# Kernel tuning notes

Hardware: AMD Instinct MI355X
Metric: run time of the kernel (lower is better)

## Reference

```python
import jax, jax.numpy as jnp
import numpy as np

C = 256
DEPTH = 4
GRIDS = [(128, 128), (128, 128), (128, 128)]
B = 2
N = 32768


def _ln_c(x, g, b):
    # LayerNorm over channel dim of [B, C, N] (myLayerNorm transposes to [B,N,C])
    m = x.mean(axis=1, keepdims=True)
    v = ((x - m) ** 2).mean(axis=1, keepdims=True)
    return (x - m) * jax.lax.rsqrt(v + 1e-5) * g[None, :, None] + b[None, :, None]


def _bn_train(x, g, b):
    # BatchNorm1d (training-mode batch stats) over [B, C, L]
    m = x.mean(axis=(0, 2), keepdims=True)
    v = ((x - m) ** 2).mean(axis=(0, 2), keepdims=True)
    return (x - m) * jax.lax.rsqrt(v + 1e-5) * g[None, :, None] + b[None, :, None]


def _dwconv3(x, w, b):
    # depthwise 3x3 conv, SAME padding; x [B,C,H,W], w [C,3,3]
    out = jax.lax.conv_general_dilated(x, w[:, None, :, :], (1, 1), 'SAME',
                                       feature_group_count=C,
                                       dimension_numbers=('NCHW', 'OIHW', 'NCHW'))
    return out + b[None, :, None, None]


def setup_inputs() -> dict:
    key = jax.random.key(0)
    ks = jax.random.split(key, 20)
    tokens = jax.random.normal(ks[0], (B, C, N), jnp.float32)
    hw = GRIDS[0][0] * GRIDS[0][1]
    cell_ind = jax.random.randint(ks[1], (B, 3, N), 0, hw)
    occupied_cell = jnp.ones((B, N), jnp.float32)

    def p(k, shape, scale=0.05):
        return scale * jax.random.normal(k, shape, jnp.float32)

    inp = dict(tokens=tokens, cell_ind=cell_ind, occupied_cell=occupied_cell)
    inp['smix_ln_g'] = 1.0 + p(ks[2], (DEPTH, C))
    inp['smix_ln_b'] = p(ks[3], (DEPTH, C))
    inp['ffn_w1'] = p(ks[4], (DEPTH, C, 3, 3), 0.2)
    inp['ffn_b1'] = p(ks[5], (DEPTH, C))
    inp['ffn_w2'] = p(ks[6], (DEPTH, C, 3, 3), 0.2)
    inp['ffn_b2'] = p(ks[7], (DEPTH, C))
    inp['att_scale'] = 1.0 + p(ks[8], (DEPTH, C))
    inp['att_bn_g'] = 1.0 + p(ks[9], (DEPTH, C))
    inp['att_bn_b'] = p(ks[10], (DEPTH, C))
    inp['cmix_ln_g'] = 1.0 + p(ks[11], (DEPTH, C))
    inp['cmix_ln_b'] = p(ks[12], (DEPTH, C))
    inp['cmix_w1'] = p(ks[13], (DEPTH, C, C), 1.0 / float(np.sqrt(C)))
    inp['cmix_b1'] = p(ks[14], (DEPTH, C))
    inp['cmix_w2'] = p(ks[15], (DEPTH, C, C), 1.0 / float(np.sqrt(C)))
    inp['cmix_b2'] = p(ks[16], (DEPTH, C))
    inp['cmix_scale'] = p(ks[17], (DEPTH, C), 0.1)
    return inp


def _forward(tokens, occupied_cell, cell_ind,
             smix_ln_g, smix_ln_b, ffn_w1, ffn_b1, ffn_w2, ffn_b2,
             att_scale, att_bn_g, att_bn_b,
             cmix_ln_g, cmix_ln_b, cmix_w1, cmix_b1, cmix_w2, cmix_b2, cmix_scale):
    Bx, Cx, Nx = tokens.shape
    bidx = jnp.arange(Bx)[:, None]
    # build_proj_matrix equivalent: per-point 1/(points-in-cell) weights + clamped indices
    sp = []
    for g in range(len(GRIDS)):
        HW = GRIDS[g][0] * GRIDS[g][1]
        ci = jnp.clip(cell_ind[:, g], 0, HW - 1)
        # inflate^T @ occupied: per-cell occupied count (occupied^2 per point)
        counts = jnp.zeros((Bx, HW), tokens.dtype).at[bidx, ci].add(occupied_cell * occupied_cell)
        # inflate @ counts: per-point count of points sharing its cell
        npp = occupied_cell * jnp.take_along_axis(counts, ci, axis=1)
        sp.append((ci, occupied_cell / (npp + 1e-6)))
    skip = [jnp.zeros(GRIDS[g], tokens.dtype) for g in range(len(GRIDS))]
    for d in range(DEPTH):
        g = d % len(GRIDS)
        H, W = GRIDS[g]
        HW = H * W
        ci, wpt = sp[g]
        # --- SpatialMix ---
        r = _ln_c(tokens, smix_ln_g[d], smix_ln_b[d]) * wpt[:, None, :]
        grid = jnp.zeros((Bx, Cx, HW), tokens.dtype).at[
            jnp.arange(Bx)[:, None, None], jnp.arange(Cx)[None, :, None], ci[:, None, :]].add(r)
        grid = grid.reshape(Bx, Cx, H, W) + skip[g]
        plane = _dwconv3(jax.nn.relu(_dwconv3(grid, ffn_w1[d], ffn_b1[d])), ffn_w2[d], ffn_b2[d])
        rflat = plane.reshape(Bx, Cx, HW)
        att = jax.nn.sigmoid(_bn_train(rflat * att_scale[d][None, :, None], att_bn_g[d], att_bn_b[d]))
        rflat = att * rflat
        r = jnp.take_along_axis(rflat, jnp.broadcast_to(ci[:, None, :], (Bx, Cx, Nx)), axis=2)
        tokens = tokens + r
        skip[g] = plane
        # --- ChannelMix ---
        h = _ln_c(tokens, cmix_ln_g[d], cmix_ln_b[d])
        h = jnp.einsum('oc,bcn->bon', cmix_w1[d], h) + cmix_b1[d][None, :, None]
        h = jnp.einsum('oc,bcn->bon', cmix_w2[d], jax.nn.relu(h)) + cmix_b2[d][None, :, None]
        tokens = tokens + h * cmix_scale[d][None, :, None]
    return tokens


def reference(tokens, cell_ind, occupied_cell,
              smix_ln_g, smix_ln_b, ffn_w1, ffn_b1, ffn_w2, ffn_b2,
              att_scale, att_bn_g, att_bn_b,
              cmix_ln_g, cmix_ln_b, cmix_w1, cmix_b1, cmix_w2, cmix_b2, cmix_scale):
    return _forward(tokens, occupied_cell, cell_ind,
                    smix_ln_g, smix_ln_b, ffn_w1, ffn_b1, ffn_w2, ffn_b2,
                    att_scale, att_bn_g, att_bn_b,
                    cmix_ln_g, cmix_ln_b, cmix_w1, cmix_b1, cmix_w2, cmix_b2, cmix_scale)
```

## Files before the change

kernel.cpp:

```cpp
#include <hip/hip_runtime.h>
#include <hip/hip_bf16.h>
#include <hip/hip_fp16.h>

#define Cc 256
#define Nn 32768
#define HWc 16384
#define Bb 2

typedef float floatx4 __attribute__((ext_vector_type(4)));
typedef short bf16x8 __attribute__((ext_vector_type(8)));
typedef unsigned short ushort8v __attribute__((ext_vector_type(8)));
typedef unsigned short ushort4v __attribute__((ext_vector_type(4)));

__device__ __forceinline__ unsigned short f2b(float f){
    unsigned u = __float_as_uint(f);
    u += 0x7fff + ((u >> 16) & 1);
    return (unsigned short)(u >> 16);
}
__device__ __forceinline__ float b2f(unsigned short h){
    return __uint_as_float(((unsigned)h) << 16);
}
__device__ __forceinline__ unsigned short f2h(float f){
    return __half_as_ushort(__float2half(f));
}
__device__ __forceinline__ float h2f(unsigned short h){
    return __half2float(__ushort_as_half(h));
}

__global__ __launch_bounds__(256) void k_count(const int* __restrict__ ci,
                                               const float* __restrict__ occ,
                                               float* __restrict__ fcounts,
                                               int* __restrict__ icounts){
    int idx = blockIdx.x*256 + threadIdx.x;
    if (idx >= Bb*3*Nn) return;
    int n = idx & (Nn-1);
    int bg = idx >> 15;
    int b = bg / 3;
    int cell = min(max(ci[idx], 0), HWc-1);
    float o = occ[(b<<15) + n];
    atomicAdd(&fcounts[(bg<<14) + cell], o*o);
    atomicAdd(&icounts[(bg<<14) + cell], 1);
}

__global__ __launch_bounds__(256) void k_wpt(const int* __restrict__ ci,
                                             const float* __restrict__ occ,
                                             const float* __restrict__ fcounts,
                                             float* __restrict__ wpt){
    int idx = blockIdx.x*256 + threadIdx.x;
    if (idx >= Bb*3*Nn) return;
    int n = idx & (Nn-1);
    int bg = idx >> 15;
    int b = bg / 3;
    int cell = min(max(ci[idx], 0), HWc-1);
    float o = occ[(b<<15) + n];
    float cnt = fcounts[(bg<<14) + cell];
    wpt[idx] = o / (o*cnt + 1e-6f);
}

__global__ __launch_bounds__(256) void k_scan(const int* __restrict__ ic,
                                              int* __restrict__ starts,
                                              int* __restrict__ cursor){
    __shared__ int part[256];
    int bg = blockIdx.x;
    int t = threadIdx.x;
    const int* cs = ic + (bg << 14);
    int base = t * 64;
    int s = 0;
    for (int i = 0; i < 64; ++i) s += cs[base + i];
    part[t] = s;
    __syncthreads();
    for (int off = 1; off < 256; off <<= 1){
        int v = (t >= off) ? part[t - off] : 0;
        __syncthreads();
        part[t] += v;
        __syncthreads();
    }
    int run = (t == 0) ? 0 : part[t - 1];
    int* st = starts + bg * (HWc + 1);
    int* cu = cursor + (bg << 14);
    for (int i = 0; i < 64; ++i){
        st[base + i] = run;
        cu[base + i] = run;
        run += cs[base + i];
    }
    if (t == 255) st[HWc] = run;
}

__global__ __launch_bounds__(256) void k_fill(const int* __restrict__ ci,
                                              int* __restrict__ cursor,
                                              int* __restrict__ plist){
    int idx = blockIdx.x*256 + threadIdx.x;
    if (idx >= Bb*3*Nn) return;
    int n = idx & (Nn-1);
    int bg = idx >> 15;
    int cell = min(max(ci[idx], 0), HWc-1);
    int pos = atomicAdd(&cursor[(bg<<14) + cell], 1);
    plist[(bg<<15) + pos] = n;
}

__global__ __launch_bounds__(256) void k_wcvt(const float* __restrict__ w1,
                                              const float* __restrict__ w2,
                                              unsigned short* __restrict__ W1b,
                                              unsigned short* __restrict__ W2b){
    int idx = blockIdx.x*256 + threadIdx.x;
    if (idx >= 4*Cc*Cc) return;
    W1b[idx] = f2b(w1[idx]);
    W2b[idx] = f2b(w2[idx]);
}

__global__ __launch_bounds__(256) void k1a_ln(const float* __restrict__ tok,
                                              const float* __restrict__ wpt,
                                              const float* __restrict__ lng,
                                              const float* __restrict__ lnb,
                                              unsigned short* __restrict__ rbuf, int g){
    __shared__ float lg[Cc], lb[Cc];
    int t = threadIdx.x;
    lg[t] = lng[t];
    lb[t] = lnb[t];
    __syncthreads();
    int b = blockIdx.x >> 7;
    int p = ((blockIdx.x & 127) << 8) + t;
    const float* tb = tok + ((size_t)b << 8)*Nn + p;
    float sum = 0.f, sq = 0.f;
    for (int c = 0; c < Cc; ++c){
        float x = tb[(size_t)c << 15];
        sum += x; sq += x*x;
    }
    float m = sum * (1.f/256.f);
    float v = sq * (1.f/256.f) - m*m;
    float r = rsqrtf(fmaxf(v, 0.f) + 1e-5f);
    float wv = wpt[(b*3 + g)*Nn + p];
    unsigned short* rb = rbuf + ((size_t)((b << 15) + p) << 8);
    for (int c0 = 0; c0 < Cc; c0 += 8){
        ushort8v u;
        #pragma unroll
        for (int j = 0; j < 8; ++j){
            int c = c0 + j;
            float x = tb[(size_t)c << 15];
            float h = ((x - m)*r*lg[c] + lb[c]) * wv;
            u[j] = f2h(h);
        }
        *(ushort8v*)(rb + c0) = u;
    }
}

__global__ __launch_bounds__(256) void k1b_gather(const unsigned short* __restrict__ rbuf,
                                                  const int* __restrict__ starts,
                                                  const int* __restrict__ plist,
                                                  unsigned short* __restrict__ grid, int g){
    int t = threadIdx.x;
    int bi = blockIdx.x;
    int b = bi >> 11;
    int cell0 = (bi & 2047) << 3;
    int bg = b*3 + g;
    const int* st = starts + bg*(HWc + 1) + cell0;
    const int* pl = plist + (bg << 15);
    const unsigned short* rb = rbuf + (((size_t)b << 15) << 8);
    float acc[8];
    int s0 = st[0];
    #pragma unroll
    for (int q = 0; q < 8; ++q){
        int s1 = st[q + 1];
        float a = 0.f;
        for (int j = s0; j < s1; ++j){
            int p = pl[j];
            a += h2f(rb[((size_t)p << 8) + t]);
        }
        acc[q] = a;
        s0 = s1;
    }
    unsigned short* go = grid + ((size_t)((b << 8) + t))*HWc + cell0;
    ushort8v u;
    #pragma unroll
    for (int e = 0; e < 8; ++e) u[e] = f2h(acc[e]);
    *(ushort8v*)go = u;
}

__global__ __launch_bounds__(256) void k2_conv(const unsigned short* __restrict__ grid,
                                               const unsigned short* __restrict__ skip,
                                               unsigned short* __restrict__ plane,
                                               const float* __restrict__ w1, const float* __restrict__ b1,
                                               const float* __restrict__ w2, const float* __restrict__ b2,
                                               const float* __restrict__ asc,
                                               float* __restrict__ bnS, float* __restrict__ bnQ,
                                               int useskip){
    __shared__ float it[36*132];
    __shared__ float mid[34*132];
    int tid = threadIdx.x;
    int bi = blockIdx.x;
    int rt = bi & 3;
    int bc = bi >> 2;
    int c = bc & 255;
    int r0 = rt << 5;
    const unsigned short* src = grid + (size_t)bc*HWc;
    const unsigned short* sk  = skip + (size_t)bc*HWc;
    for (int i = tid; i < 36; i += 256){
        it[i*132 + 0] = 0.f; it[i*132 + 1] = 0.f;
        it[i*132 + 130] = 0.f; it[i*132 + 131] = 0.f;
    }
    for (int i = tid; i < 36*16; i += 256){
        int r = i >> 4, ch = i & 15;
        int gy = r0 - 2 + r;
        float vals[8];
        #pragma unroll
        for (int e = 0; e < 8; ++e) vals[e] = 0.f;
        if ((unsigned)gy < 128u){
            ushort8v sv = *(const ushort8v*)(src + (gy << 7) + ch*8);
            if (useskip){
                ushort8v kv = *(const ushort8v*)(sk + (gy << 7) + ch*8);
                #pragma unroll
                for (int e = 0; e < 8; ++e) vals[e] = h2f(sv[e]) + h2f(kv[e]);
            } else {
                #pragma unroll
                for (int e = 0; e < 8; ++e) vals[e] = h2f(sv[e]);
            }
        }
        #pragma unroll
        for (int e = 0; e < 8; ++e) it[r*132 + 2 + ch*8 + e] = vals[e];
    }
    float a1[9], a2[9];
    #pragma unroll
    for (int j = 0; j < 9; ++j){ a1[j] = w1[c*9+j]; a2[j] = w2[c*9+j]; }
    float bb1 = b1[c], bb2 = b2[c], sc = asc[c];
    __syncthreads();
    for (int i = tid; i < 34*130; i += 256){
        int r = i / 130, cc = i - r*130;
        int y = r0 - 1 + r, x = cc - 1;
        float v = 0.f;
        if ((unsigned)y < 128u && (unsigned)x < 128u){
            float s = 0.f;
            #pragma unroll
            for (int j = 0; j < 9; ++j) s += a1[j] * it[(r + j/3)*132 + cc + (j%3)];
            v = fmaxf(s + bb1, 0.f);
        }
        mid[r*132 + cc] = v;
    }
    __syncthreads();
    float ps = 0.f, pq = 0.f;
    unsigned short* dst = plane + (size_t)bc*HWc;
    for (int i = tid; i < 32*32; i += 256){
        int yy = i >> 5, ch = i & 31;
        int x0 = ch << 2;
        ushort4v u;
        #pragma unroll
        for (int e = 0; e < 4; ++e){
            int x = x0 + e;
            float s = 0.f;
            #pragma unroll
            for (int j = 0; j < 9; ++j) s += a2[j] * mid[(yy + j/3)*132 + x + (j%3)];
            float v = s + bb2;
            u[e] = f2h(v);
            float t = v * sc;
            ps += t; pq += t*t;
        }
        *(ushort4v*)(dst + ((r0 + yy) << 7) + x0) = u;
    }
    __syncthreads();
    it[tid] = ps; it[256 + tid] = pq;
    __syncthreads();
    for (int s2 = 128; s2 > 0; s2 >>= 1){
        if (tid < s2){ it[tid] += it[tid+s2]; it[256+tid] += it[256+tid+s2]; }
        __syncthreads();
    }
    if (tid == 0){
        atomicAdd(&bnS[c], it[0]);
        atomicAdd(&bnQ[c], it[256]);
    }
}

__global__ __launch_bounds__(256) void k3t_att_t(const unsigned short* __restrict__ plane,
                                                 const float* __restrict__ bnS, const float* __restrict__ bnQ,
                                                 const float* __restrict__ asc,
                                                 const float* __restrict__ bng, const float* __restrict__ bnb,
                                                 unsigned short* __restrict__ attp){
    __shared__ float t[32*33];
    __shared__ float P_s[32], Q_s[32];
    int tid = threadIdx.x;
    int tx = tid & 31, ty = tid >> 5;
    int bi = blockIdx.x;
    int ht = bi & 511;
    int ct = (bi >> 9) & 7;
    int b  = bi >> 12;
    int c0 = ct << 5, h0 = ht << 5;
    if (tid < 32){
        int c = c0 + tid;
        float mean = bnS[c] * (1.f/32768.f);
        float var  = bnQ[c] * (1.f/32768.f) - mean*mean;
        float inv  = rsqrtf(fmaxf(var, 0.f) + 1e-5f) * bng[c];
        P_s[tid] = asc[c] * inv;
        Q_s[tid] = bnb[c] - mean * inv;
    }
    __syncthreads();
    for (int r = ty; r < 32; r += 8){
        int c = c0 + r;
        float v = h2f(plane[(((size_t)b << 8) + c)*HWc + h0 + tx]);
        float s = 1.f / (1.f + __expf(-(P_s[r]*v + Q_s[r])));
        t[r*33 + tx] = s * v;
    }
    __syncthreads();
    for (int r = ty; r < 32; r += 8){
        attp[(((size_t)b << 14) + h0 + r)*Cc + c0 + tx] = f2h(t[tx*33 + r]);
    }
}

__global__ __launch_bounds__(512, 4) void k4_cmix(const float* __restrict__ tsrc, int tin_nc,
                                               float* __restrict__ tdst, int tout_nc,
                                               const unsigned short* __restrict__ attp,
                                               const int* __restrict__ ci,
                                               const unsigned short* __restrict__ W1,
                                               const unsigned short* __restrict__ W2,
                                               const float* __restrict__ lng, const float* __restrict__ lnb,
                                               const float* __restrict__ b1, const float* __restrict__ b2,
                                               const float* __restrict__ csc,
                                               const float* __restrict__ lng2, const float* __restrict__ lnb2,
                                               const float* __restrict__ wptb,
                                               unsigned short* __restrict__ rbufn,
                                               int g, int g2, int donext){
    __shared__ __align__(16) unsigned short hs[64*264];
    __shared__ float reds[512], redq[512];
    __shared__ float m_s[64], r_s[64];
    __shared__ int cell_s[64];
    __shared__ float lng_s[Cc], lnb_s[Cc], b1_s[Cc], b2s_s[Cc], cs_s[Cc], g2g_s[Cc], g2b_s[Cc];

    int tid = threadIdx.x;
    int bi = blockIdx.x;
    int b = bi >> 9;
    int p0 = (bi & 511) << 6;

    if (tid < 256){
        lng_s[tid] = lng[tid];
        lnb_s[tid] = lnb[tid];
        b1_s[tid]  = b1[tid];
        float cv = csc[tid];
        cs_s[tid]  = cv;
        b2s_s[tid] = b2[tid] * cv;
        g2g_s[tid] = lng2[tid];
        g2b_s[tid] = lnb2[tid];
    }
    if (tid < 64){
        int cc = ci[(b*3 + g)*Nn + p0 + tid];
        cell_s[tid] = min(max(cc, 0), HWc-1);
    }
    __syncthreads();

    int p  = tid & 63;
    int cg = tid >> 6;
    int c0 = cg << 5;

    const unsigned short* ar = attp + ((size_t)((b << 14) + cell_s[p]))*Cc + c0;
    ushort8v rr[4];
    #pragma unroll
    for (int j = 0; j < 4; ++j) rr[j] = *(const ushort8v*)(ar + 8*j);

    float vreg[32];
    float sum = 0.f, sq = 0.f;
    if (tin_nc){
        const floatx4* tn4 = (const floatx4*)(tsrc + ((((size_t)(b << 15)) + p0 + p) << 8) + c0);
        #pragma unroll
        for (int j = 0; j < 8; ++j){
            floatx4 f = tn4[j];
            #pragma unroll
            for (int e = 0; e < 4; ++e){
                int k = j*4 + e;
                float v = f[e] + h2f(rr[k >> 3][k & 7]);
                vreg[k] = v; sum += v; sq += v*v;
            }
        }
    } else {
        const float* tb = tsrc + ((size_t)b << 8)*Nn + p0 + p;
        #pragma unroll
        for (int k = 0; k < 32; ++k){
            float v = tb[(size_t)(c0 + k) << 15] + h2f(rr[k >> 3][k & 7]);
            vreg[k] = v; sum += v; sq += v*v;
        }
    }
    reds[tid] = sum; redq[tid] = sq;
    __syncthreads();
    if (tid < 64){
        float s = 0.f, q = 0.f;
        #pragma unroll
        for (int j = 0; j < 8; ++j){ s += reds[j*64 + tid]; q += redq[j*64 + tid]; }
        float m = s * (1.f/256.f);
        float var = q * (1.f/256.f) - m*m;
        m_s[tid] = m;
        r_s[tid] = rsqrtf(fmaxf(var, 0.f) + 1e-5f);
    }
    __syncthreads();
    float mp = m_s[p], rp = r_s[p];
    unsigned short* hrow = &hs[p*264 + c0];
    #pragma unroll
    for (int j = 0; j < 4; ++j){
        ushort8v u;
        #pragma unroll
        for (int e = 0; e < 8; ++e){
            int k = j*8 + e, c = c0 + k;
            u[e] = f2b((vreg[k] - mp)*rp*lng_s[c] + lnb_s[c]);
        }
        *(ushort8v*)(hrow + 8*j) = u;
    }
    __syncthreads();

    int lane = tid & 63;
    int w = tid >> 6;
    int l15 = lane & 15;
    int q4 = lane >> 4;
    floatx4 acc[2][4];
    #pragma unroll
    for (int mi = 0; mi < 2; ++mi)
        #pragma unroll
        for (int ni = 0; ni < 4; ++ni)
            acc[mi][ni] = (floatx4){0.f, 0.f, 0.f, 0.f};

    #pragma unroll
    for (int kk = 0; kk < 8; ++kk){
        int k0 = kk*32 + q4*8;
        bf16x8 bfr[4];
        #pragma unroll
        for (int ni = 0; ni < 4; ++ni)
            bfr[ni] = *(const bf16x8*)&hs[(ni*16 + l15)*264 + k0];
        #pragma unroll
        for (int mi = 0; mi < 2; ++mi){
            bf16x8 af = *(const bf16x8*)&W1[(size_t)(w*32 + mi*16 + l15)*Cc + k0];
            #pragma unroll
            for (int ni = 0; ni < 4; ++ni)
                acc[mi][ni] = __builtin_amdgcn_mfma_f32_16x16x32_bf16(af, bfr[ni], acc[mi][ni], 0, 0, 0);
        }
    }
    __syncthreads();
    #pragma unroll
    for (int mi = 0; mi < 2; ++mi)
        #pragma unroll
        for (int ni = 0; ni < 4; ++ni){
            int m0 = w*32 + mi*16 + q4*4;
            int nn = ni*16 + l15;
            ushort4v u;
            #pragma unroll
            for (int r = 0; r < 4; ++r)
                u[r] = f2b(fmaxf(acc[mi][ni][r] + b1_s[m0 + r], 0.f));
            *(ushort4v*)&hs[nn*264 + m0] = u;
        }
    __syncthreads();

    #pragma unroll
    for (int mi = 0; mi < 2; ++mi)
        #pragma unroll
        for (int ni = 0; ni < 4; ++ni)
            acc[mi][ni] = (floatx4){0.f, 0.f, 0.f, 0.f};
    #pragma unroll
    for (int kk = 0; kk < 8; ++kk){
        int k0 = kk*32 + q4*8;
        bf16x8 bfr[4];
        #pragma unroll
        for (int ni = 0; ni < 4; ++ni)
            bfr[ni] = *(const bf16x8*)&hs[(ni*16 + l15)*264 + k0];
        #pragma unroll
        for (int mi = 0; mi < 2; ++mi){
            bf16x8 af = *(const bf16x8*)&W2[(size_t)(w*32 + mi*16 + l15)*Cc + k0];
            #pragma unroll
            for (int ni = 0; ni < 4; ++ni)
                acc[mi][ni] = __builtin_amdgcn_mfma_f32_16x16x32_bf16(af, bfr[ni], acc[mi][ni], 0, 0, 0);
        }
    }
    __syncthreads();
    #pragma unroll
    for (int mi = 0; mi < 2; ++mi)
        #pragma unroll
        for (int ni = 0; ni < 4; ++ni){
            int m0 = w*32 + mi*16 + q4*4;
            int nn = ni*16 + l15;
            ushort4v u;
            #pragma unroll
            for (int r = 0; r < 4; ++r)
                u[r] = f2b(acc[mi][ni][r]*cs_s[m0 + r] + b2s_s[m0 + r]);
            *(ushort4v*)&hs[nn*264 + m0] = u;
        }
    __syncthreads();

    float sum2 = 0.f, sq2 = 0.f;
    if (tout_nc){
        float* tn = tdst + ((((size_t)(b << 15)) + p0 + p) << 8) + c0;
        #pragma unroll
        for (int j = 0; j < 4; ++j){
            ushort8v u = *(const ushort8v*)(hrow + 8*j);
            floatx4 fa, fb;
            #pragma unroll
            for (int e = 0; e < 4; ++e){
                int k = j*8 + e;
                float v = vreg[k] + b2f(u[e]);
                vreg[k] = v; fa[e] = v; sum2 += v; sq2 += v*v;
            }
            #pragma unroll
            for (int e = 4; e < 8; ++e){
                int k = j*8 + e;
                float v = vreg[k] + b2f(u[e]);
                vreg[k] = v; fb[e-4] = v; sum2 += v; sq2 += v*v;
            }
            *(floatx4*)(tn + 8*j) = fa;
            *(floatx4*)(tn + 8*j + 4) = fb;
        }
    } else {
        float* ob = tdst + ((size_t)b << 8)*Nn + p0 + p;
        #pragma unroll
        for (int j = 0; j < 4; ++j){
            ushort8v u = *(const ushort8v*)(hrow + 8*j);
            #pragma unroll
            for (int e = 0; e < 8; ++e){
                int k = j*8 + e, c = c0 + k;
                float v = vreg[k] + b2f(u[e]);
                vreg[k] = v;
                ob[(size_t)c << 15] = v;
                sum2 += v; sq2 += v*v;
            }
        }
    }
    if (donext){
        reds[tid] = sum2; redq[tid] = sq2;
        __syncthreads();
        if (tid < 64){
            float s = 0.f, q = 0.f;
            #pragma unroll
            for (int j = 0; j < 8; ++j){ s += reds[j*64 + tid]; q += redq[j*64 + tid]; }
            float m = s * (1.f/256.f);
            float var = q * (1.f/256.f) - m*m;
            m_s[tid] = m;
            r_s[tid] = rsqrtf(fmaxf(var, 0.f) + 1e-5f);
        }
        __syncthreads();
        float m2 = m_s[p], rr2 = r_s[p];
        float wv2 = wptb[(b*3 + g2)*Nn + p0 + p];
        unsigned short* rb = rbufn + ((size_t)((b << 15) + p0 + p))*Cc + c0;
        #pragma unroll
        for (int j = 0; j < 4; ++j){
            ushort8v u;
            #pragma unroll
            for (int e = 0; e < 8; ++e){
                int k = j*8 + e, c = c0 + k;
                u[e] = f2h(((vreg[k] - m2)*rr2*g2g_s[c] + g2b_s[c]) * wv2);
            }
            *(ushort8v*)(rb + 8*j) = u;
        }
    }
}

extern "C" void kernel_launch(void* const* d_in, const int* in_sizes, int n_in,
                              void* d_out, int out_size, void* d_ws, size_t ws_size,
                              hipStream_t stream){
    (void)in_sizes; (void)n_in; (void)out_size;
    const float* tokens  = (const float*)d_in[0];
    const int*   cellind = (const int*)d_in[1];
    const float* occ     = (const float*)d_in[2];
    const float* smix_g  = (const float*)d_in[3];
    const float* smix_b  = (const float*)d_in[4];
    const float* ffn_w1  = (const float*)d_in[5];
    const float* ffn_b1  = (const float*)d_in[6];
    const float* ffn_w2  = (const float*)d_in[7];
    const float* ffn_b2  = (const float*)d_in[8];
    const float* att_sc  = (const float*)d_in[9];
    const float* bn_g    = (const float*)d_in[10];
    const float* bn_b    = (const float*)d_in[11];
    const float* cm_g    = (const float*)d_in[12];
    const float* cm_b    = (const float*)d_in[13];
    const float* cw1     = (const float*)d_in[14];
    const float* cb1     = (const float*)d_in[15];
    const float* cw2     = (const float*)d_in[16];
    const float* cb2     = (const float*)d_in[17];
    const float* cscale  = (const float*)d_in[18];
    float* out = (float*)d_out;
    char* w = (char*)d_ws;

    const size_t HGRID_BYTES = (size_t)Bb*Cc*HWc*2;
    unsigned short* grid_h  = (unsigned short*)(w);
    unsigned short* attp_h  = grid_h;
    unsigned short* planeA  = (unsigned short*)(w + HGRID_BYTES);
    unsigned short* planeB  = (unsigned short*)(w + 2*HGRID_BYTES);
    unsigned short* rbuf    = (unsigned short*)(w + 3*HGRID_BYTES);
    size_t o = 3*HGRID_BYTES + (size_t)Bb*Nn*Cc*2;
    float* fcounts = (float*)(w + o); o += (size_t)Bb*3*HWc*4;
    int*   icounts = (int*)(w + o);   o += (size_t)Bb*3*HWc*4;
    float* wptb   = (float*)(w + o); o += (size_t)Bb*3*Nn*4;
    float* bnS    = (float*)(w + o);
    float* bnQ    = bnS + 256;
    o += 4096;
    unsigned short* W1b = (unsigned short*)(w + o);
    unsigned short* W2b = W1b + 4*Cc*Cc;
    o += (size_t)2*4*Cc*Cc*2;
    int* startsb  = (int*)(w + o); o += (size_t)Bb*3*(HWc+1)*4;
    int* cursors  = (int*)(w + o); o += (size_t)Bb*3*HWc*4;
    int* plistb   = (int*)(w + o); o += (size_t)Bb*3*Nn*4;
    o = (o + 255) & ~(size_t)255;
    float* tnc    = (float*)(w + o);
    size_t needed = o + (size_t)Bb*Nn*Cc*4;
    int nc_ok = (ws_size >= needed) ? 1 : 0;

    hipMemsetAsync(fcounts, 0, (size_t)2*Bb*3*HWc*4, stream);
    k_count<<<(Bb*3*Nn)/256, 256, 0, stream>>>(cellind, occ, fcounts, icounts);
    k_wpt<<<(Bb*3*Nn)/256, 256, 0, stream>>>(cellind, occ, fcounts, wptb);
    k_scan<<<Bb*3, 256, 0, stream>>>(icounts, startsb, cursors);
    k_fill<<<(Bb*3*Nn)/256, 256, 0, stream>>>(cellind, cursors, plistb);
    k_wcvt<<<(4*Cc*Cc)/256, 256, 0, stream>>>(cw1, cw2, W1b, W2b);

    k1a_ln<<<Bb*(Nn/256), 256, 0, stream>>>(tokens, wptb, smix_g, smix_b, rbuf, 0);

    for (int d = 0; d < 4; ++d){
        int g = d % 3;
        int g2 = (d + 1) % 3;
        int donext = (d < 3) ? 1 : 0;
        int useskip = (d == 3) ? 1 : 0;
        unsigned short* plane = (d == 0) ? planeA : planeB;
        int dn = (d + 1 < 4) ? d + 1 : d;

        const float* tsrc; int tin_nc;
        float* tdst; int tout_nc;
        if (nc_ok){
            tsrc = (d == 0) ? tokens : tnc;  tin_nc  = (d == 0) ? 0 : 1;
            tdst = (d == 3) ? out : tnc;     tout_nc = (d == 3) ? 0 : 1;
        } else {
            tsrc = (d == 0) ? tokens : out;  tin_nc  = 0;
            tdst = out;                      tout_nc = 0;
        }

        hipMemsetAsync(bnS, 0, 2048, stream);

        k1b_gather<<<Bb*(HWc/8), 256, 0, stream>>>(rbuf, startsb, plistb, grid_h, g);
        k2_conv<<<Bb*Cc*4, 256, 0, stream>>>(grid_h, planeA, plane,
                                             ffn_w1 + d*Cc*9, ffn_b1 + d*Cc,
                                             ffn_w2 + d*Cc*9, ffn_b2 + d*Cc,
                                             att_sc + d*Cc, bnS, bnQ, useskip);
        k3t_att_t<<<Bb*8*512, 256, 0, stream>>>(plane, bnS, bnQ, att_sc + d*Cc,
                                                bn_g + d*Cc, bn_b + d*Cc, attp_h);
        k4_cmix<<<Bb*(Nn/64), 512, 0, stream>>>(tsrc, tin_nc, tdst, tout_nc, attp_h, cellind,
                                                W1b + (size_t)d*Cc*Cc, W2b + (size_t)d*Cc*Cc,
                                                cm_g + d*Cc, cm_b + d*Cc,
                                                cb1 + d*Cc, cb2 + d*Cc, cscale + d*Cc,
                                                smix_g + dn*Cc, smix_b + dn*Cc, wptb,
                                                rbuf, g, g2, donext);
    }
}
```

Baseline: 757.1 us.

## Split LN across channel groups, vectorize depthwise conv, fold BN-stat zeroing into gather

The initial LayerNorm kernel now runs 512 threads per 64 positions. Each thread loads 32 channels into registers once and the statistics are reduced through shared memory, so the old two-pass reload of tokens is gone. The depthwise 3x3 convolutions compute four outputs per thread from vector LDS reads, with the row stride padded to 136. The separate memset of the BN sum buffers is removed; block 0 of the gather kernel zeroes them instead. This relies on stream ordering and adds register pressure in the LN kernel.

```diff
diff --git a/kernel.cpp b/kernel.cpp
--- a/kernel.cpp
+++ b/kernel.cpp
@@ -108,48 +108,65 @@
     W2b[idx] = f2b(w2[idx]);
 }
 
-__global__ __launch_bounds__(256) void k1a_ln(const float* __restrict__ tok,
+__global__ __launch_bounds__(512, 4) void k1a_ln(const float* __restrict__ tok,
                                               const float* __restrict__ wpt,
                                               const float* __restrict__ lng,
                                               const float* __restrict__ lnb,
                                               unsigned short* __restrict__ rbuf, int g){
+    __shared__ float reds[512], redq[512];
+    __shared__ float m_s[64], r_s[64];
     __shared__ float lg[Cc], lb[Cc];
-    int t = threadIdx.x;
-    lg[t] = lng[t];
-    lb[t] = lnb[t];
-    __syncthreads();
-    int b = blockIdx.x >> 7;
-    int p = ((blockIdx.x & 127) << 8) + t;
-    const float* tb = tok + ((size_t)b << 8)*Nn + p;
+    int tid = threadIdx.x;
+    int bi = blockIdx.x;
+    int b = bi >> 9;
+    int p0 = (bi & 511) << 6;
+    if (tid < 256){ lg[tid] = lng[tid]; lb[tid] = lnb[tid]; }
+    int p  = tid & 63;
+    int cg = tid >> 6;
+    int c0 = cg << 5;
+    const float* tb = tok + ((size_t)b << 8)*Nn + p0 + p;
+    float vreg[32];
     float sum = 0.f, sq = 0.f;
-    for (int c = 0; c < Cc; ++c){
-        float x = tb[(size_t)c << 15];
-        sum += x; sq += x*x;
-    }
-    float m = sum * (1.f/256.f);
-    float v = sq * (1.f/256.f) - m*m;
-    float r = rsqrtf(fmaxf(v, 0.f) + 1e-5f);
-    float wv = wpt[(b*3 + g)*Nn + p];
-    unsigned short* rb = rbuf + ((size_t)((b << 15) + p) << 8);
-    for (int c0 = 0; c0 < Cc; c0 += 8){
+    #pragma unroll
+    for (int k = 0; k < 32; ++k){
+        float v = tb[(size_t)(c0 + k) << 15];
+        vreg[k] = v; sum += v; sq += v*v;
+    }
+    reds[tid] = sum; redq[tid] = sq;
+    __syncthreads();
+    if (tid < 64){
+        float s = 0.f, q = 0.f;
+        #pragma unroll
+        for (int j = 0; j < 8; ++j){ s += reds[j*64 + tid]; q += redq[j*64 + tid]; }
+        float m = s * (1.f/256.f);
+        float var = q * (1.f/256.f) - m*m;
+        m_s[tid] = m;
+        r_s[tid] = rsqrtf(fmaxf(var, 0.f) + 1e-5f);
+    }
+    __syncthreads();
+    float mp = m_s[p], rp = r_s[p];
+    float wv = wpt[(b*3 + g)*Nn + p0 + p];
+    unsigned short* rb = rbuf + ((size_t)((b << 15) + p0 + p))*Cc + c0;
+    #pragma unroll
+    for (int j = 0; j < 4; ++j){
         ushort8v u;
         #pragma unroll
-        for (int j = 0; j < 8; ++j){
-            int c = c0 + j;
-            float x = tb[(size_t)c << 15];
-            float h = ((x - m)*r*lg[c] + lb[c]) * wv;
-            u[j] = f2h(h);
-        }
-        *(ushort8v*)(rb + c0) = u;
+        for (int e = 0; e < 8; ++e){
+            int k = j*8 + e, c = c0 + k;
+            u[e] = f2h(((vreg[k] - mp)*rp*lg[c] + lb[c]) * wv);
+        }
+        *(ushort8v*)(rb + 8*j) = u;
     }
 }
 
 __global__ __launch_bounds__(256) void k1b_gather(const unsigned short* __restrict__ rbuf,
                                                   const int* __restrict__ starts,
                                                   const int* __restrict__ plist,
-                                                  unsigned short* __restrict__ grid, int g){
+                                                  unsigned short* __restrict__ grid,
+                                                  float* __restrict__ bnSQ, int g){
     int t = threadIdx.x;
     int bi = blockIdx.x;
+    if (bi == 0){ bnSQ[t] = 0.f; bnSQ[256 + t] = 0.f; }
     int b = bi >> 11;
     int cell0 = (bi & 2047) << 3;
     int bg = b*3 + g;
@@ -184,8 +201,8 @@
                                                const float* __restrict__ asc,
                                                float* __restrict__ bnS, float* __restrict__ bnQ,
                                                int useskip){
-    __shared__ float it[36*132];
-    __shared__ float mid[34*132];
+    __shared__ float it[36*136];
+    __shared__ float mid[34*136];
     int tid = threadIdx.x;
     int bi = blockIdx.x;
     int rt = bi & 3;
@@ -195,8 +212,9 @@
     const unsigned short* src = grid + (size_t)bc*HWc;
     const unsigned short* sk  = skip + (size_t)bc*HWc;
     for (int i = tid; i < 36; i += 256){
-        it[i*132 + 0] = 0.f; it[i*132 + 1] = 0.f;
-        it[i*132 + 130] = 0.f; it[i*132 + 131] = 0.f;
+        it[i*136 + 0] = 0.f;   it[i*136 + 1] = 0.f;
+        it[i*136 + 130] = 0.f; it[i*136 + 131] = 0.f;
+        it[i*136 + 132] = 0.f; it[i*136 + 133] = 0.f;
     }
     for (int i = tid; i < 36*16; i += 256){
         int r = i >> 4, ch = i & 15;
@@ -216,44 +234,63 @@
             }
         }
         #pragma unroll
-        for (int e = 0; e < 8; ++e) it[r*132 + 2 + ch*8 + e] = vals[e];
+        for (int e = 0; e < 8; ++e) it[r*136 + 2 + ch*8 + e] = vals[e];
     }
     float a1[9], a2[9];
     #pragma unroll
     for (int j = 0; j < 9; ++j){ a1[j] = w1[c*9+j]; a2[j] = w2[c*9+j]; }
     float bb1 = b1[c], bb2 = b2[c], sc = asc[c];
     __syncthreads();
-    for (int i = tid; i < 34*130; i += 256){
-        int r = i / 130, cc = i - r*130;
-        int y = r0 - 1 + r, x = cc - 1;
-        float v = 0.f;
-        if ((unsigned)y < 128u && (unsigned)x < 128u){
-            float s = 0.f;
-            #pragma unroll
-            for (int j = 0; j < 9; ++j) s += a1[j] * it[(r + j/3)*132 + cc + (j%3)];
-            v = fmaxf(s + bb1, 0.f);
-        }
-        mid[r*132 + cc] = v;
+    for (int i = tid; i < 34*33; i += 256){
+        int r = i / 33, chk = i - r*33;
+        int cc0 = chk << 2;
+        int y = r0 - 1 + r;
+        bool yok = (unsigned)y < 128u;
+        float o0 = 0.f, o1 = 0.f, o2 = 0.f, o3 = 0.f;
+        if (yok){
+            #pragma unroll
+            for (int jr = 0; jr < 3; ++jr){
+                const float* row = &it[(r + jr)*136 + cc0];
+                floatx4 a = *(const floatx4*)row;
+                float a4 = row[4], a5 = row[5];
+                float w0 = a1[jr*3+0], w1v = a1[jr*3+1], w2v = a1[jr*3+2];
+                o0 += w0*a[0] + w1v*a[1] + w2v*a[2];
+                o1 += w0*a[1] + w1v*a[2] + w2v*a[3];
+                o2 += w0*a[2] + w1v*a[3] + w2v*a4;
+                o3 += w0*a[3] + w1v*a4  + w2v*a5;
+            }
+        }
+        float* mrow = &mid[r*136 + cc0];
+        mrow[0] = (yok && cc0+0 >= 1 && cc0+0 <= 128) ? fmaxf(o0 + bb1, 0.f) : 0.f;
+        mrow[1] = (yok && cc0+1 >= 1 && cc0+1 <= 128) ? fmaxf(o1 + bb1, 0.f) : 0.f;
+        mrow[2] = (yok && cc0+2 >= 1 && cc0+2 <= 128) ? fmaxf(o2 + bb1, 0.f) : 0.f;
+        mrow[3] = (yok && cc0+3 >= 1 && cc0+3 <= 128) ? fmaxf(o3 + bb1, 0.f) : 0.f;
     }
     __syncthreads();
     float ps = 0.f, pq = 0.f;
     unsigned short* dst = plane + (size_t)bc*HWc;
     for (int i = tid; i < 32*32; i += 256){
-        int yy = i >> 5, ch = i & 31;
-        int x0 = ch << 2;
+        int yy = i >> 5, chk = i & 31;
+        int x0 = chk << 2;
+        float o0 = 0.f, o1 = 0.f, o2 = 0.f, o3 = 0.f;
+        #pragma unroll
+        for (int jr = 0; jr < 3; ++jr){
+            const float* row = &mid[(yy + jr)*136 + x0];
+            floatx4 a = *(const floatx4*)row;
+            float a4 = row[4], a5 = row[5];
+            float w0 = a2[jr*3+0], w1v = a2[jr*3+1], w2v = a2[jr*3+2];
+            o0 += w0*a[0] + w1v*a[1] + w2v*a[2];
+            o1 += w0*a[1] + w1v*a[2] + w2v*a[3];
+            o2 += w0*a[2] + w1v*a[3] + w2v*a4;
+            o3 += w0*a[3] + w1v*a4  + w2v*a5;
+        }
+        float v0 = o0 + bb2, v1 = o1 + bb2, v2 = o2 + bb2, v3 = o3 + bb2;
         ushort4v u;
-        #pragma unroll
-        for (int e = 0; e < 4; ++e){
-            int x = x0 + e;
-            float s = 0.f;
-            #pragma unroll
-            for (int j = 0; j < 9; ++j) s += a2[j] * mid[(yy + j/3)*132 + x + (j%3)];
-            float v = s + bb2;
-            u[e] = f2h(v);
-            float t = v * sc;
-            ps += t; pq += t*t;
-        }
+        u[0] = f2h(v0); u[1] = f2h(v1); u[2] = f2h(v2); u[3] = f2h(v3);
         *(ushort4v*)(dst + ((r0 + yy) << 7) + x0) = u;
+        float t0 = v0*sc, t1 = v1*sc, t2 = v2*sc, t3 = v3*sc;
+        ps += t0 + t1 + t2 + t3;
+        pq += t0*t0 + t1*t1 + t2*t2 + t3*t3;
     }
     __syncthreads();
     it[tid] = ps; it[256 + tid] = pq;
@@ -599,7 +636,7 @@
     k_fill<<<(Bb*3*Nn)/256, 256, 0, stream>>>(cellind, cursors, plistb);
     k_wcvt<<<(4*Cc*Cc)/256, 256, 0, stream>>>(cw1, cw2, W1b, W2b);
 
-    k1a_ln<<<Bb*(Nn/256), 256, 0, stream>>>(tokens, wptb, smix_g, smix_b, rbuf, 0);
+    k1a_ln<<<Bb*(Nn/64), 512, 0, stream>>>(tokens, wptb, smix_g, smix_b, rbuf, 0);
 
     for (int d = 0; d < 4; ++d){
         int g = d % 3;
@@ -619,9 +656,7 @@
             tdst = out;                      tout_nc = 0;
         }
 
-        hipMemsetAsync(bnS, 0, 2048, stream);
-
-        k1b_gather<<<Bb*(HWc/8), 256, 0, stream>>>(rbuf, startsb, plistb, grid_h, g);
+        k1b_gather<<<Bb*(HWc/8), 256, 0, stream>>>(rbuf, startsb, plistb, grid_h, bnS, g);
         k2_conv<<<Bb*Cc*4, 256, 0, stream>>>(grid_h, planeA, plane,
                                              ffn_w1 + d*Cc*9, ffn_b1 + d*Cc,
                                              ffn_w2 + d*Cc*9, ffn_b2 + d*Cc,
```

Result: faster. 702.9 us (-7.2%).
